# Kernel tuning notes

Hardware: AMD Instinct MI355X
Metric: run time of the kernel (lower is better)

Reference implementation:

```python
import jax, jax.numpy as jnp
import numpy as np

B, N, DIM = 2, 2048, 512
H, DH = 8, 64
INNER = H * DH
SCALE = DH ** -0.5


def setup_inputs() -> dict:
    key = jax.random.key(0)
    ks = jax.random.split(key, 8)
    s = 0.02
    return {
        "nodes": jax.random.normal(ks[0], (B, N, DIM), dtype=jnp.float32),
        "edge_mask": jax.random.bernoulli(ks[1], 0.9, (B, N, N)),
        "wq": jax.random.normal(ks[2], (DIM, INNER), dtype=jnp.float32) * s,
        "bq": jnp.zeros((INNER,), dtype=jnp.float32),
        "wkv": jax.random.normal(ks[3], (DIM, 2 * INNER), dtype=jnp.float32) * s,
        "bkv": jnp.zeros((2 * INNER,), dtype=jnp.float32),
        "wo": jax.random.normal(ks[4], (INNER, DIM), dtype=jnp.float32) * s,
        "bo": jnp.zeros((DIM,), dtype=jnp.float32),
    }


def reference(nodes, edge_mask, wq, bq, wkv, bkv, wo, bo):
    b, n, _ = nodes.shape
    q = nodes @ wq + bq                      # [b, n, h*dh]
    kv = nodes @ wkv + bkv                   # [b, n, 2*h*dh]
    k, v = jnp.split(kv, 2, axis=-1)
    # split heads -> [b, h, n, dh]
    split = lambda t: t.reshape(b, n, H, DH).transpose(0, 2, 1, 3)
    q, k, v = split(q), split(k), split(v)
    sim = jnp.einsum('bhid,bhjd->bhij', q, k) * SCALE
    max_neg = -jnp.finfo(sim.dtype).max
    sim = jnp.where(edge_mask[:, None, :, :], sim, max_neg)
    attn = jax.nn.softmax(sim, axis=-1)
    out = jnp.einsum('bhij,bhjd->bhid', attn, v)      # [b, h, n, dh]
    out = out.transpose(0, 2, 1, 3).reshape(b, n, INNER)
    return out @ wo + bo
```

## Files before the change

### kernel.cpp

```cpp
#include <hip/hip_runtime.h>
#include <cstdint>
#include <cstddef>

#define DEVI __device__ __forceinline__

typedef __bf16 bf16x8 __attribute__((ext_vector_type(8)));
typedef __bf16 bf16x2 __attribute__((ext_vector_type(2)));
typedef float floatx4 __attribute__((ext_vector_type(4)));
typedef unsigned short us4v __attribute__((ext_vector_type(4)));
typedef unsigned short us8 __attribute__((ext_vector_type(8)));

static_assert(sizeof(bf16x8) == 16, "bf16x8 must be 16B");


#if __has_builtin(__builtin_amdgcn_cvt_pk_bf16_f32)
DEVI unsigned short f2bf(float f) {
  union { bf16x2 v; unsigned short u[2]; } c;
  c.v = __builtin_amdgcn_cvt_pk_bf16_f32(f, 0.f);
  return c.u[0];
}
DEVI unsigned int pk2bf(float a, float b) {
  union { bf16x2 v; unsigned int u; } c;
  c.v = __builtin_amdgcn_cvt_pk_bf16_f32(a, b);
  return c.u;
}
#else
DEVI unsigned short f2bf(float f) {
  unsigned int u = __float_as_uint(f);
  u += 0x7fffu + ((u >> 16) & 1u);
  return (unsigned short)(u >> 16);
}
DEVI unsigned int pk2bf(float a, float b) {
  return (unsigned int)f2bf(a) | ((unsigned int)f2bf(b) << 16);
}
#endif

DEVI float exp2c(float x) {
#if __has_builtin(__builtin_amdgcn_exp2f)
  return __builtin_amdgcn_exp2f(x);
#else
  return exp2f(x);
#endif
}

DEVI bf16x8 ld8(const unsigned short* p) { return *(const bf16x8*)p; }

typedef const __attribute__((address_space(1))) void* gas_ptr;
typedef __attribute__((address_space(3))) void* las_ptr;

DEVI void gld16(const void* g, void* l) {
  __builtin_amdgcn_global_load_lds((gas_ptr)g, (las_ptr)l, 16, 0, 0);
}

#define WAIT_LGKM0() __builtin_amdgcn_s_waitcnt(0xc07f)

__global__ __launch_bounds__(256) void prep_k(
    const float* __restrict__ nodes, const void* __restrict__ mask,
    const float* __restrict__ wq, const float* __restrict__ wkv,
    const float* __restrict__ wo,
    unsigned short* __restrict__ XB, unsigned short* __restrict__ WQKVT,
    unsigned short* __restrict__ WOT, unsigned int* __restrict__ pm) {
  int bid = blockIdx.x;
  if (bid < 8192) {
    __shared__ int mode;
    const unsigned int* md = (const unsigned int*)mask;
    unsigned int probe = md[threadIdx.x];
    bool odd = (probe > 1u && probe != 0x3f800000u);
    if (threadIdx.x == 0) mode = 0;
    __syncthreads();
    if (odd) atomicOr(&mode, 1);
    __syncthreads();
    int byteMode = mode;
    int t = bid * 256 + threadIdx.x;
    int lane = threadIdx.x & 63;
    unsigned int n;
    if (byteMode) {
      unsigned int x = md[t];
      n = ((x & 0xffu) ? 1u : 0u) | ((x & 0xff00u) ? 2u : 0u) |
          ((x & 0xff0000u) ? 4u : 0u) | ((x >> 24) ? 8u : 0u);
    } else {
      uint4 v = ((const uint4*)mask)[t];
      n = (v.x ? 1u : 0u) | (v.y ? 2u : 0u) | (v.z ? 4u : 0u) | (v.w ? 8u : 0u);
    }
    unsigned int w = n << ((lane & 7) * 4);
    w |= __shfl_xor(w, 1);
    w |= __shfl_xor(w, 2);
    w |= __shfl_xor(w, 4);
    if ((lane & 7) == 0) pm[t >> 3] = w;
  } else if (bid < 10240) {
    int i = (bid - 8192) * 256 + threadIdx.x;
    float4 v = ((const float4*)nodes)[i];
    us4v o;
    o[0] = f2bf(v.x); o[1] = f2bf(v.y); o[2] = f2bf(v.z); o[3] = f2bf(v.w);
    *(us4v*)(XB + (size_t)i * 4) = o;
  } else {
    int tb = bid - 10240;
    int x = tb & 15, y = (tb >> 4) & 7, z = tb >> 7;
    const float* src; unsigned short* dst; int C, c0;
    if (z == 0)      { if (x >= 8) return; src = wq;  dst = WQKVT; C = 512;  c0 = 0; }
    else if (z == 1) { src = wkv; dst = WQKVT; C = 1024; c0 = 512; }
    else             { if (x >= 8) return; src = wo;  dst = WOT;  C = 512;  c0 = 0; }
    __shared__ unsigned short t2[64 * 64];
    const int t = threadIdx.x;
    const int ct = x * 64, rt = y * 64;
    for (int p = 0; p < 4; p++) {
      int kl = p * 16 + (t >> 4);
      int cc = (t & 15) * 4;
      float4 v = *(const float4*)&src[(size_t)(rt + kl) * C + ct + cc];
      float f[4] = {v.x, v.y, v.z, v.w};
      for (int i = 0; i < 4; i++) {
        int c = cc + i;
        t2[c * 64 + (kl ^ (c & 56))] = f2bf(f[i]);
      }
    }
    __syncthreads();
    for (int p = 0; p < 2; p++) {
      int c = p * 32 + (t >> 3);
      int kc = (t & 7) * 8;
      us8 v = *(const us8*)&t2[c * 64 + (kc ^ (c & 56))];
      *(us8*)&dst[(size_t)(c0 + ct + c) * 512 + rt + kc] = v;
    }
  }
}

__global__ __launch_bounds__(256) void gemm_qkv_k(
    const unsigned short* __restrict__ A,
    const unsigned short* __restrict__ Bt,
    const float* __restrict__ bq, const float* __restrict__ bkv,
    unsigned short* __restrict__ Qo, unsigned short* __restrict__ Ko,
    unsigned short* __restrict__ VTo) {
  __shared__ unsigned short smem[12288];
  const int tid = threadIdx.x;
  const int wave = tid >> 6, lane = tid & 63, quad = lane >> 4, l16 = lane & 15;
  const int wm = wave >> 1, wn = wave & 1;
  const int bm = blockIdx.x, bn = blockIdx.y;
  floatx4 acc[2][4] = {};
  const int arow = lane >> 2;
  const int ag = lane & 3;

  auto stage = [&](int kt, int buf) {
    unsigned short* sA = smem + buf * 6144;
    unsigned short* sB = sA + 2048;
    int rowA = wave * 16 + arow;
    int gA = ag ^ (rowA & 3);
    gld16(&A[(size_t)(bm * 64 + rowA) * 512 + kt * 32 + gA * 8], &sA[(wave * 16) * 32]);
    for (int p = 0; p < 2; p++) {
      int rowB = p * 64 + wave * 16 + arow;
      int gB = ag ^ (rowB & 3);
      gld16(&Bt[(size_t)(bn * 128 + rowB) * 512 + kt * 32 + gB * 8],
            &sB[(p * 64 + wave * 16) * 32]);
    }
  };

  stage(0, 0);
  for (int kt = 0; kt < 16; kt++) {
    __syncthreads();
    if (kt + 1 < 16) stage(kt + 1, (kt + 1) & 1);
    const unsigned short* sA = smem + (kt & 1) * 6144;
    const unsigned short* sB = sA + 2048;
    bf16x8 aF[2], bF[4];
    int swz = (quad ^ (l16 & 3)) * 8;
    for (int i = 0; i < 2; i++) aF[i] = ld8(&sA[(wm * 32 + i * 16 + l16) * 32 + swz]);
    for (int j = 0; j < 4; j++) bF[j] = ld8(&sB[(wn * 64 + j * 16 + l16) * 32 + swz]);
    for (int i = 0; i < 2; i++)
      for (int j = 0; j < 4; j++)
        acc[i][j] = __builtin_amdgcn_mfma_f32_16x16x32_bf16(aF[i], bF[j], acc[i][j], 0, 0, 0);
  }

  const int sec = bn * 2 + wn;
  float bias[4];
  float scale = 1.0f;
  if (sec < 8) {
    for (int j = 0; j < 4; j++) bias[j] = bq[sec * 64 + j * 16 + l16];
    scale = 0.18033688011112042f;
  } else {
    for (int j = 0; j < 4; j++) bias[j] = bkv[(sec - 8) * 64 + j * 16 + l16];
  }
  const int gr0 = bm * 64 + wm * 32;
  const int b = gr0 >> 11, n0 = gr0 & 2047;
  unsigned short* pw = smem + wave * 2048;
  __syncthreads();
  if (sec < 16) {
    for (int i = 0; i < 2; i++)
      for (int j = 0; j < 4; j++) {
        int cg = j * 2 + (l16 >> 3), ci = l16 & 7;
        for (int r = 0; r < 4; r++) {
          int row = i * 16 + quad * 4 + r;
          pw[row * 64 + ((cg ^ (row & 7)) * 8) + ci] = f2bf((acc[i][j][r] + bias[j]) * scale);
        }
      }
    WAIT_LGKM0();
    unsigned short* dst = (sec < 8) ? Qo + ((size_t)(b * 8 + sec) * 2048 + n0) * 64
                                    : Ko + ((size_t)(b * 8 + sec - 8) * 2048 + n0) * 64;
    for (int p = 0; p < 4; p++) {
      int row = p * 8 + (lane >> 3);
      int c8 = lane & 7;
      us8 v = *(const us8*)&pw[row * 64 + ((c8 ^ (row & 7)) * 8)];
      *(us8*)&dst[(size_t)row * 64 + c8 * 8] = v;
    }
  } else {
    for (int i = 0; i < 2; i++)
      for (int j = 0; j < 4; j++) {
        int d = j * 16 + l16;
        us4v t;
        for (int r = 0; r < 4; r++) t[r] = f2bf(acc[i][j][r] + bias[j]);
        *(us4v*)&pw[d * 32 + ((quad ^ (d & 3)) * 8) + i * 4] = t;
      }
    WAIT_LGKM0();
    unsigned short* dst = VTo + (size_t)(b * 8 + sec - 16) * 64 * 2048 + n0;
    for (int p = 0; p < 4; p++) {
      int d = p * 16 + (lane >> 2);
      int c4 = lane & 3;
      us8 v = *(const us8*)&pw[d * 32 + ((c4 ^ (d & 3)) * 8)];
      *(us8*)&dst[(size_t)d * 2048 + c4 * 8] = v;
    }
  }
}

__global__ __launch_bounds__(256, 2) void attn_k(
    const unsigned short* __restrict__ Q,
    const unsigned short* __restrict__ K,
    const unsigned short* __restrict__ Vt,
    const unsigned int* __restrict__ pm,
    unsigned short* __restrict__ AO) {
  __shared__ unsigned short smem[32768];
  __shared__ float lsumB[4][64];
  const int tid = threadIdx.x;
  const int wave = tid >> 6, lane = tid & 63, quad = lane >> 4, l16 = lane & 15;
  const int bh = blockIdx.x, qt = blockIdx.y, b = bh >> 3, h = bh & 7;
  const int q0 = qt * 64;
  const unsigned short* Qb = Q + (size_t)bh * 2048 * 64;
  const unsigned short* Kb = K + (size_t)bh * 2048 * 64;
  const unsigned short* Vb = Vt + (size_t)bh * 64 * 2048;
  const unsigned int* pmB = pm + (size_t)b * 2048 * 64;

  bf16x8 qF[4][2];
  for (int qb = 0; qb < 4; qb++) {
    qF[qb][0] = ld8(&Qb[(size_t)(q0 + qb * 16 + l16) * 64 + quad * 8]);
    qF[qb][1] = ld8(&Qb[(size_t)(q0 + qb * 16 + l16) * 64 + 32 + quad * 8]);
  }

  floatx4 oacc[4][4] = {};
  float lsum[4] = {0.f, 0.f, 0.f, 0.f};

  const int krow = lane >> 3;
  const int kg = (lane & 7) ^ krow;
  const int vrow = lane >> 2;
  const int vpos = lane & 3;

  auto stage = [&](int it, int buf) {
    const int k0w = it * 128 + wave * 32;
    unsigned short* kTw = smem + buf * 16384 + wave * 2048;
    unsigned short* vTw = smem + buf * 16384 + 8192 + wave * 2048;
    for (int p = 0; p < 4; p++) {
      int row = p * 8 + krow;
      gld16(&Kb[(size_t)(k0w + row) * 64 + kg * 8], &kTw[p * 512]);
      int d = p * 16 + vrow;
      int gsrc = vpos ^ ((d >> 1) & 3);
      gld16(&Vb[(size_t)d * 2048 + k0w + gsrc * 8], &vTw[p * 512]);
    }
  };

  stage(0, 0);
  const int rsw0 = quad ^ (l16 & 7);
  const int rsw1 = (4 + quad) ^ (l16 & 7);

  for (int it = 0; it < 16; ++it) {
    const int buf = it & 1;
    __syncthreads();
    if (it + 1 < 16) stage(it + 1, buf ^ 1);

    const unsigned short* kTw = smem + buf * 16384 + wave * 2048;
    const unsigned short* vTw = smem + buf * 16384 + 8192 + wave * 2048;

    unsigned int mw[4];
    for (int qb = 0; qb < 4; qb++)
      mw[qb] = pmB[(size_t)(q0 + qb * 16 + l16) * 64 + it * 4 + wave];

    floatx4 st[4][2];
    for (int k2 = 0; k2 < 2; k2++) {
      const unsigned short* kr = &kTw[(k2 * 16 + l16) * 64];
      bf16x8 kf0 = ld8(kr + rsw0 * 8);
      bf16x8 kf1 = ld8(kr + rsw1 * 8);
      for (int qb = 0; qb < 4; qb++) {
        floatx4 z = {0.f, 0.f, 0.f, 0.f};
        z = __builtin_amdgcn_mfma_f32_16x16x32_bf16(kf0, qF[qb][0], z, 0, 0, 0);
        st[qb][k2] = __builtin_amdgcn_mfma_f32_16x16x32_bf16(kf1, qF[qb][1], z, 0, 0, 0);
      }
    }

    union uB { bf16x8 v; unsigned int d[4]; } pf[4];
    for (int qb = 0; qb < 4; qb++) {
      unsigned int w = mw[qb];
      for (int k2 = 0; k2 < 2; k2++) {
        int base = k2 * 16 + quad * 4;
        float e0 = exp2c(st[qb][k2][0]); e0 = ((w >> (base + 0)) & 1u) ? e0 : 0.f;
        float e1 = exp2c(st[qb][k2][1]); e1 = ((w >> (base + 1)) & 1u) ? e1 : 0.f;
        float e2 = exp2c(st[qb][k2][2]); e2 = ((w >> (base + 2)) & 1u) ? e2 : 0.f;
        float e3 = exp2c(st[qb][k2][3]); e3 = ((w >> (base + 3)) & 1u) ? e3 : 0.f;
        lsum[qb] += (e0 + e1) + (e2 + e3);
        pf[qb].d[k2 * 2]     = pk2bf(e0, e1);
        pf[qb].d[k2 * 2 + 1] = pk2bf(e2, e3);
      }
    }

    for (int db = 0; db < 4; db++) {
      int row = db * 16 + l16;
      int pos = quad ^ ((row >> 1) & 3);
      bf16x8 va = ld8(&vTw[row * 32 + pos * 8]);
      for (int qb = 0; qb < 4; qb++)
        oacc[db][qb] =
            __builtin_amdgcn_mfma_f32_16x16x32_bf16(va, pf[qb].v, oacc[db][qb], 0, 0, 0);
    }
  }
  __syncthreads();

  for (int qb = 0; qb < 4; qb++) {
    lsum[qb] += __shfl_xor(lsum[qb], 16);
    lsum[qb] += __shfl_xor(lsum[qb], 32);
  }
  lsumB[wave][quad * 16 + l16] = lsum[quad];

  float* pO = (float*)smem;
  float* myR = pO + wave * 4096;
  for (int db = 0; db < 4; db++)
    for (int qb = 0; qb < 4; qb++) {
      int q = qb * 16 + l16;
      *(floatx4*)&myR[q * 64 + (((db * 4 + quad) ^ l16) & 15) * 4] = oacc[db][qb];
    }
  __syncthreads();
  {
    int q = tid >> 2, dblk = tid & 3;
    float inv = 1.0f / (lsumB[0][q] + lsumB[1][q] + lsumB[2][q] + lsumB[3][q]);
    float o[16];
    for (int i = 0; i < 4; i++) {
      int dg = dblk * 4 + i;
      int off = q * 64 + ((dg ^ q) & 15) * 4;
      floatx4 s = *(floatx4*)&pO[off];
      s += *(floatx4*)&pO[4096 + off];
      s += *(floatx4*)&pO[8192 + off];
      s += *(floatx4*)&pO[12288 + off];
      for (int r = 0; r < 4; r++) o[i * 4 + r] = s[r] * inv;
    }
    us8 v0, v1;
    for (int i = 0; i < 8; i++) { v0[i] = f2bf(o[i]); v1[i] = f2bf(o[8 + i]); }
    unsigned short* dst = &AO[((size_t)b * 2048 + q0 + q) * 512 + h * 64 + dblk * 16];
    *(us8*)dst = v0;
    *(us8*)(dst + 8) = v1;
  }
}

__global__ __launch_bounds__(256) void gemm_out_k(
    const unsigned short* __restrict__ A,
    const unsigned short* __restrict__ Bt,
    const float* __restrict__ bo, float* __restrict__ out) {
  __shared__ unsigned short smem[12288];
  const int tid = threadIdx.x;
  const int wave = tid >> 6, lane = tid & 63, quad = lane >> 4, l16 = lane & 15;
  const int wm = wave >> 1, wn = wave & 1;
  const int bm = blockIdx.x, bn = blockIdx.y;
  floatx4 acc[2][4] = {};
  const int arow = lane >> 2;
  const int ag = lane & 3;

  auto stage = [&](int kt, int buf) {
    unsigned short* sA = smem + buf * 6144;
    unsigned short* sB = sA + 2048;
    int rowA = wave * 16 + arow;
    int gA = ag ^ (rowA & 3);
    gld16(&A[(size_t)(bm * 64 + rowA) * 512 + kt * 32 + gA * 8], &sA[(wave * 16) * 32]);
    for (int p = 0; p < 2; p++) {
      int rowB = p * 64 + wave * 16 + arow;
      int gB = ag ^ (rowB & 3);
      gld16(&Bt[(size_t)(bn * 128 + rowB) * 512 + kt * 32 + gB * 8],
            &sB[(p * 64 + wave * 16) * 32]);
    }
  };

  stage(0, 0);
  for (int kt = 0; kt < 16; kt++) {
    __syncthreads();
    if (kt + 1 < 16) stage(kt + 1, (kt + 1) & 1);
    const unsigned short* sA = smem + (kt & 1) * 6144;
    const unsigned short* sB = sA + 2048;
    bf16x8 aF[2], bF[4];
    int swz = (quad ^ (l16 & 3)) * 8;
    for (int i = 0; i < 2; i++) aF[i] = ld8(&sA[(wm * 32 + i * 16 + l16) * 32 + swz]);
    for (int j = 0; j < 4; j++) bF[j] = ld8(&sB[(wn * 64 + j * 16 + l16) * 32 + swz]);
    for (int i = 0; i < 2; i++)
      for (int j = 0; j < 4; j++)
        acc[i][j] = __builtin_amdgcn_mfma_f32_16x16x32_bf16(aF[i], bF[j], acc[i][j], 0, 0, 0);
  }
  for (int i = 0; i < 2; i++)
    for (int j = 0; j < 4; j++) {
      int gc = bn * 128 + wn * 64 + j * 16 + l16;
      float bb = bo[gc];
      for (int r = 0; r < 4; r++) {
        int gr = bm * 64 + wm * 32 + i * 16 + quad * 4 + r;
        out[(size_t)gr * 512 + gc] = acc[i][j][r] + bb;
      }
    }
}

extern "C" void kernel_launch(void* const* d_in, const int* in_sizes, int n_in,
                              void* d_out, int out_size, void* d_ws, size_t ws_size,
                              hipStream_t stream) {
  const float* nodes = (const float*)d_in[0];
  const void*  mask  = d_in[1];
  const float* wq    = (const float*)d_in[2];
  const float* bq    = (const float*)d_in[3];
  const float* wkv   = (const float*)d_in[4];
  const float* bkv   = (const float*)d_in[5];
  const float* wo    = (const float*)d_in[6];
  const float* bo    = (const float*)d_in[7];
  float* out = (float*)d_out;

  char* ws = (char*)d_ws;
  unsigned short* XB    = (unsigned short*)(ws + 0);
  unsigned short* WQKVT = (unsigned short*)(ws + 4194304);
  unsigned short* WOT   = (unsigned short*)(ws + 5767168);
  unsigned short* Qm    = (unsigned short*)(ws + 6291456);
  unsigned short* Km    = (unsigned short*)(ws + 10485760);
  unsigned short* VTm   = (unsigned short*)(ws + 18874368);
  unsigned short* AOm   = (unsigned short*)(ws + 23068672);
  unsigned int*   PM    = (unsigned int*)(ws + 27262976);

  prep_k<<<10624, 256, 0, stream>>>(nodes, mask, wq, wkv, wo, XB, WQKVT, WOT, PM);
  gemm_qkv_k<<<dim3(64, 12), 256, 0, stream>>>(XB, WQKVT, bq, bkv, Qm, Km, VTm);
  attn_k<<<dim3(16, 32), 256, 0, stream>>>(Qm, Km, VTm, PM, AOm);
  gemm_out_k<<<dim3(64, 4), 256, 0, stream>>>(AOm, WOT, bo, out);
}
```

Measured before the change: 156.1 us.

## Load K/V fragments directly from global, shrink LDS, raise attention occupancy

The attention kernel no longer stages K and V tiles through double-buffered LDS with async copies. Each wave now loads its MFMA fragments straight from global memory, which removes the per-iteration block barriers. The packed mask is relaid out so each wave's words for one query row are contiguous. The partial-output reduction is serialized through a single 16KB LDS buffer, which lets launch bounds go to 3 blocks per SM. The trade is uncoalesced, unswizzled global loads and no prefetch overlap, plus four barriers in the epilogue.

```diff
diff --git a/kernel.cpp b/kernel.cpp
--- a/kernel.cpp
+++ b/kernel.cpp
@@ -86,7 +86,12 @@
     w |= __shfl_xor(w, 1);
     w |= __shfl_xor(w, 2);
     w |= __shfl_xor(w, 4);
-    if ((lane & 7) == 0) pm[t >> 3] = w;
+    if ((lane & 7) == 0) {
+      unsigned int lin = (unsigned int)(t >> 3);
+      unsigned int q_lin = lin >> 6;
+      unsigned int word = lin & 63;
+      pm[(q_lin * 4 + (word & 3)) * 16 + (word >> 2)] = w;
+    }
   } else if (bid < 10240) {
     int i = (bid - 8192) * 256 + threadIdx.x;
     float4 v = ((const float4*)nodes)[i];
@@ -217,13 +222,13 @@
   }
 }
 
-__global__ __launch_bounds__(256, 2) void attn_k(
+__global__ __launch_bounds__(256, 3) void attn_k(
     const unsigned short* __restrict__ Q,
     const unsigned short* __restrict__ K,
     const unsigned short* __restrict__ Vt,
     const unsigned int* __restrict__ pm,
     unsigned short* __restrict__ AO) {
-  __shared__ unsigned short smem[32768];
+  __shared__ float Ored[4096];
   __shared__ float lsumB[4][64];
   const int tid = threadIdx.x;
   const int wave = tid >> 6, lane = tid & 63, quad = lane >> 4, l16 = lane & 15;
@@ -232,7 +237,6 @@
   const unsigned short* Qb = Q + (size_t)bh * 2048 * 64;
   const unsigned short* Kb = K + (size_t)bh * 2048 * 64;
   const unsigned short* Vb = Vt + (size_t)bh * 64 * 2048;
-  const unsigned int* pmB = pm + (size_t)b * 2048 * 64;
 
   bf16x8 qF[4][2];
   for (int qb = 0; qb < 4; qb++) {
@@ -240,80 +244,52 @@
     qF[qb][1] = ld8(&Qb[(size_t)(q0 + qb * 16 + l16) * 64 + 32 + quad * 8]);
   }
 
+  size_t mbase[4];
+  for (int qb = 0; qb < 4; qb++)
+    mbase[qb] = ((size_t)(b * 2048 + q0 + qb * 16 + l16) * 4 + wave) * 16;
+
   floatx4 oacc[4][4] = {};
   float lsum[4] = {0.f, 0.f, 0.f, 0.f};
 
-  const int krow = lane >> 3;
-  const int kg = (lane & 7) ^ krow;
-  const int vrow = lane >> 2;
-  const int vpos = lane & 3;
-
-  auto stage = [&](int it, int buf) {
+  for (int it = 0; it < 16; ++it) {
     const int k0w = it * 128 + wave * 32;
-    unsigned short* kTw = smem + buf * 16384 + wave * 2048;
-    unsigned short* vTw = smem + buf * 16384 + 8192 + wave * 2048;
-    for (int p = 0; p < 4; p++) {
-      int row = p * 8 + krow;
-      gld16(&Kb[(size_t)(k0w + row) * 64 + kg * 8], &kTw[p * 512]);
-      int d = p * 16 + vrow;
-      int gsrc = vpos ^ ((d >> 1) & 3);
-      gld16(&Vb[(size_t)d * 2048 + k0w + gsrc * 8], &vTw[p * 512]);
-    }
-  };
-
-  stage(0, 0);
-  const int rsw0 = quad ^ (l16 & 7);
-  const int rsw1 = (4 + quad) ^ (l16 & 7);
-
-  for (int it = 0; it < 16; ++it) {
-    const int buf = it & 1;
-    __syncthreads();
-    if (it + 1 < 16) stage(it + 1, buf ^ 1);
-
-    const unsigned short* kTw = smem + buf * 16384 + wave * 2048;
-    const unsigned short* vTw = smem + buf * 16384 + 8192 + wave * 2048;
+
+    bf16x8 va[4];
+    for (int db = 0; db < 4; db++)
+      va[db] = ld8(&Vb[(size_t)(db * 16 + l16) * 2048 + k0w + quad * 8]);
 
     unsigned int mw[4];
-    for (int qb = 0; qb < 4; qb++)
-      mw[qb] = pmB[(size_t)(q0 + qb * 16 + l16) * 64 + it * 4 + wave];
-
-    floatx4 st[4][2];
+    for (int qb = 0; qb < 4; qb++) mw[qb] = pm[mbase[qb] + it];
+
+    union uB { bf16x8 v; unsigned int d[4]; } pf[4];
     for (int k2 = 0; k2 < 2; k2++) {
-      const unsigned short* kr = &kTw[(k2 * 16 + l16) * 64];
-      bf16x8 kf0 = ld8(kr + rsw0 * 8);
-      bf16x8 kf1 = ld8(kr + rsw1 * 8);
+      const unsigned short* kr = &Kb[(size_t)(k0w + k2 * 16 + l16) * 64 + quad * 8];
+      bf16x8 kf0 = ld8(kr);
+      bf16x8 kf1 = ld8(kr + 32);
+      floatx4 st[4];
       for (int qb = 0; qb < 4; qb++) {
         floatx4 z = {0.f, 0.f, 0.f, 0.f};
         z = __builtin_amdgcn_mfma_f32_16x16x32_bf16(kf0, qF[qb][0], z, 0, 0, 0);
-        st[qb][k2] = __builtin_amdgcn_mfma_f32_16x16x32_bf16(kf1, qF[qb][1], z, 0, 0, 0);
-      }
-    }
-
-    union uB { bf16x8 v; unsigned int d[4]; } pf[4];
-    for (int qb = 0; qb < 4; qb++) {
-      unsigned int w = mw[qb];
-      for (int k2 = 0; k2 < 2; k2++) {
+        st[qb] = __builtin_amdgcn_mfma_f32_16x16x32_bf16(kf1, qF[qb][1], z, 0, 0, 0);
+      }
+      for (int qb = 0; qb < 4; qb++) {
+        unsigned int w = mw[qb];
         int base = k2 * 16 + quad * 4;
-        float e0 = exp2c(st[qb][k2][0]); e0 = ((w >> (base + 0)) & 1u) ? e0 : 0.f;
-        float e1 = exp2c(st[qb][k2][1]); e1 = ((w >> (base + 1)) & 1u) ? e1 : 0.f;
-        float e2 = exp2c(st[qb][k2][2]); e2 = ((w >> (base + 2)) & 1u) ? e2 : 0.f;
-        float e3 = exp2c(st[qb][k2][3]); e3 = ((w >> (base + 3)) & 1u) ? e3 : 0.f;
+        float e0 = exp2c(st[qb][0]); e0 = ((w >> (base + 0)) & 1u) ? e0 : 0.f;
+        float e1 = exp2c(st[qb][1]); e1 = ((w >> (base + 1)) & 1u) ? e1 : 0.f;
+        float e2 = exp2c(st[qb][2]); e2 = ((w >> (base + 2)) & 1u) ? e2 : 0.f;
+        float e3 = exp2c(st[qb][3]); e3 = ((w >> (base + 3)) & 1u) ? e3 : 0.f;
         lsum[qb] += (e0 + e1) + (e2 + e3);
         pf[qb].d[k2 * 2]     = pk2bf(e0, e1);
         pf[qb].d[k2 * 2 + 1] = pk2bf(e2, e3);
       }
     }
 
-    for (int db = 0; db < 4; db++) {
-      int row = db * 16 + l16;
-      int pos = quad ^ ((row >> 1) & 3);
-      bf16x8 va = ld8(&vTw[row * 32 + pos * 8]);
+    for (int db = 0; db < 4; db++)
       for (int qb = 0; qb < 4; qb++)
         oacc[db][qb] =
-            __builtin_amdgcn_mfma_f32_16x16x32_bf16(va, pf[qb].v, oacc[db][qb], 0, 0, 0);
-    }
-  }
-  __syncthreads();
+            __builtin_amdgcn_mfma_f32_16x16x32_bf16(va[db], pf[qb].v, oacc[db][qb], 0, 0, 0);
+  }
 
   for (int qb = 0; qb < 4; qb++) {
     lsum[qb] += __shfl_xor(lsum[qb], 16);
@@ -321,14 +297,24 @@
   }
   lsumB[wave][quad * 16 + l16] = lsum[quad];
 
-  float* pO = (float*)smem;
-  float* myR = pO + wave * 4096;
-  for (int db = 0; db < 4; db++)
-    for (int qb = 0; qb < 4; qb++) {
-      int q = qb * 16 + l16;
-      *(floatx4*)&myR[q * 64 + (((db * 4 + quad) ^ l16) & 15) * 4] = oacc[db][qb];
-    }
-  __syncthreads();
+  for (int w = 0; w < 4; w++) {
+    if (wave == w) {
+      for (int db = 0; db < 4; db++)
+        for (int qb = 0; qb < 4; qb++) {
+          int q = qb * 16 + l16;
+          int off = q * 64 + (((db * 4 + quad) ^ l16) & 15) * 4;
+          if (w == 0) {
+            *(floatx4*)&Ored[off] = oacc[db][qb];
+          } else {
+            floatx4 t = *(floatx4*)&Ored[off];
+            t += oacc[db][qb];
+            *(floatx4*)&Ored[off] = t;
+          }
+        }
+    }
+    __syncthreads();
+  }
+
   {
     int q = tid >> 2, dblk = tid & 3;
     float inv = 1.0f / (lsumB[0][q] + lsumB[1][q] + lsumB[2][q] + lsumB[3][q]);
@@ -336,10 +322,7 @@
     for (int i = 0; i < 4; i++) {
       int dg = dblk * 4 + i;
       int off = q * 64 + ((dg ^ q) & 15) * 4;
-      floatx4 s = *(floatx4*)&pO[off];
-      s += *(floatx4*)&pO[4096 + off];
-      s += *(floatx4*)&pO[8192 + off];
-      s += *(floatx4*)&pO[12288 + off];
+      floatx4 s = *(floatx4*)&Ored[off];
       for (int r = 0; r < 4; r++) o[i * 4 + r] = s[r] * inv;
     }
     us8 v0, v1;
```

Measured after the change: 199.0 us. 1.27x slower.
